# Optimization experiments

Hardware: AMD Instinct MI355X
Metric: run time of the kernel (lower is better)

## Reference

```python
import jax, jax.numpy as jnp
import numpy as np

B, L, D, H = 4, 2048, 1024, 16
DH = D // H

def setup_inputs() -> dict:
    key = jax.random.key(0)
    ks = jax.random.split(key, 9)
    s = 1.0 / np.sqrt(D)
    x = jax.random.normal(ks[0], (B, L, D), dtype=jnp.float32)
    Wq = jax.random.uniform(ks[1], (D, D), jnp.float32, -s, s)
    bq = jax.random.uniform(ks[2], (D,), jnp.float32, -s, s)
    Wk = jax.random.uniform(ks[3], (D, D), jnp.float32, -s, s)
    bk = jax.random.uniform(ks[4], (D,), jnp.float32, -s, s)
    Wv = jax.random.uniform(ks[5], (D, D), jnp.float32, -s, s)
    bv = jax.random.uniform(ks[6], (D,), jnp.float32, -s, s)
    Wo = jax.random.uniform(ks[7], (D, D), jnp.float32, -s, s)
    bo = jax.random.uniform(ks[8], (D,), jnp.float32, -s, s)
    mask = jnp.tril(jnp.ones((L, L), dtype=jnp.int32))[None, None]  # [1,1,L,L] causal
    return {"x": x, "Wq": Wq, "bq": bq, "Wk": Wk, "bk": bk, "Wv": Wv, "bv": bv,
            "Wo": Wo, "bo": bo, "mask": mask}

def reference(x, Wq, bq, Wk, bk, Wv, bv, Wo, bo, mask):
    # projections (torch Linear: x @ W.T + b; here W stored transposed already as [D,D])
    q = (x @ Wq + bq).reshape(B, L, H, DH).transpose(0, 2, 1, 3)  # [B,H,L,Dh]
    k = (x @ Wk + bk).reshape(B, L, H, DH).transpose(0, 2, 1, 3)
    v = (x @ Wv + bv).reshape(B, L, H, DH).transpose(0, 2, 1, 3)
    scores = jnp.einsum('bhqd,bhkd->bhqk', q, k) / jnp.sqrt(jnp.float32(DH))
    scores = jnp.where(mask == 0, -jnp.inf, scores)
    attn = jax.nn.softmax(scores, axis=-1)
    out = jnp.einsum('bhqk,bhkd->bhqd', attn, v)  # [B,H,L,Dh]
    out = out.transpose(0, 2, 1, 3).reshape(B, L, D)
    return out @ Wo + bo
```

## Files before the change

### kernel.cpp

```cpp
#include <hip/hip_runtime.h>
#include <hip/hip_bf16.h>


typedef __bf16 bf16;
typedef __bf16 bf16x4 __attribute__((ext_vector_type(4)));
typedef __bf16 bf16x8 __attribute__((ext_vector_type(8)));
typedef float f32x4 __attribute__((ext_vector_type(4)));

#define DEV static __device__ __forceinline__

constexpr int B = 4, L = 2048, D = 1024, H = 16, DH = 64;
constexpr int BL = B * L;
constexpr int GM = 8192, GK = 1024;
constexpr int BKg = 64;

typedef __attribute__((address_space(1))) const void* gptr1;
typedef __attribute__((address_space(3))) void* lptr3;

DEV void load_lds16(const bf16* g, bf16* l) {
  __builtin_amdgcn_global_load_lds((gptr1)g, (lptr3)l, 16, 0, 0);
}

DEV f32x4 mfma(bf16x8 a, bf16x8 b, f32x4 c) {
  return __builtin_amdgcn_mfma_f32_16x16x32_bf16(a, b, c, 0, 0, 0);
}

DEV float scrub(float v) { return (v == v) ? v : 0.f; }
DEV float max3f(float a, float b, float c) { return fmaxf(fmaxf(a, b), c); }

__global__ void sniff_k(const unsigned short* __restrict__ xr, int* flag) {
  __shared__ int cnt;
  if (threadIdx.x == 0) cnt = 0;
  __syncthreads();
  int local = 0;
  for (int i = threadIdx.x; i < 4096; i += 256) {
    const unsigned short u = xr[2 * i];
    const int e = (u >> 7) & 0xFF;
    if (e >= 0x70 && e <= 0x85) local++;
  }
  atomicAdd(&cnt, local);
  __syncthreads();
  if (threadIdx.x == 0) *flag = (cnt > 2048) ? 1 : 0;
}

__global__ __launch_bounds__(256) void cvt_x_k(const void* __restrict__ src,
                                               bf16* __restrict__ dst,
                                               const int* __restrict__ flag, int n) {
  const bool isbf = (*flag != 0);
  const int stride = gridDim.x * blockDim.x * 8;
  for (int idx = (blockIdx.x * blockDim.x + threadIdx.x) * 8; idx < n; idx += stride) {
    bf16x8 o;
    if (isbf) {
      bf16x8 v = *(const bf16x8*)((const bf16*)src + idx);
      #pragma unroll
      for (int j = 0; j < 8; ++j) o[j] = (bf16)scrub((float)v[j]);
    } else {
      const float* s = (const float*)src + idx;
      #pragma unroll
      for (int j = 0; j < 8; ++j) o[j] = (bf16)scrub(s[j]);
    }
    *(bf16x8*)&dst[idx] = o;
  }
}

__global__ __launch_bounds__(256) void wtrans_cvt4_k(const void* __restrict__ W0,
                                                     const void* __restrict__ W1,
                                                     const void* __restrict__ W2,
                                                     const void* __restrict__ W3,
                                                     bf16* __restrict__ dstBase,
                                                     const int* __restrict__ flag) {
  __shared__ bf16 t[32][33];
  const bool isbf = (*flag != 0);
  const int z = blockIdx.z;
  const void* src = (z == 0) ? W0 : (z == 1) ? W1 : (z == 2) ? W2 : W3;
  bf16* dst = dstBase + (size_t)z * D * D;
  const int bx = blockIdx.x * 32, by = blockIdx.y * 32;
  const int tx = threadIdx.x & 31, ty = threadIdx.x >> 5;
  for (int i = ty; i < 32; i += 8) {
    const size_t off = (size_t)(by + i) * D + bx + tx;
    const float v = isbf ? (float)((const bf16*)src)[off] : ((const float*)src)[off];
    t[i][tx] = (bf16)scrub(v);
  }
  __syncthreads();
  for (int i = ty; i < 32; i += 8)
    dst[(size_t)(bx + i) * D + by + tx] = t[tx][i];
}

__global__ __launch_bounds__(256) void qkv_gemm_k(const bf16* __restrict__ A,
                                                  const bf16* __restrict__ Bt,
                                                  const void* __restrict__ bq,
                                                  const void* __restrict__ bk,
                                                  const void* __restrict__ bv,
                                                  bf16* __restrict__ Q,
                                                  bf16* __restrict__ Kk,
                                                  bf16* __restrict__ VT,
                                                  const int* __restrict__ flag) {
  __shared__ __align__(16) bf16 As[128 * BKg];
  __shared__ __align__(16) bf16 Bs[128 * BKg];
  const bool isbf = (*flag != 0);
  const int wg = blockIdx.x;
  const int local = wg >> 3;
  const int mt = (wg & 7) * 8 + (local & 7);
  const int nt = local >> 3;
  const int m0 = mt * 128, n0 = nt * 128;
  const int buf = n0 >> 10, nloc = n0 & 1023;
  const void* bias = (buf == 0) ? bq : (buf == 1) ? bk : bv;
  const float scale = (buf == 0) ? 0.18033688011111f : 1.0f;

  const int tid = threadIdx.x, wave = tid >> 6, lane = tid & 63;
  const int wr = wave >> 1, wc = wave & 1;
  const int quad = lane >> 4, l16 = lane & 15;
  const int srow = lane >> 3;
  const int scol = ((lane ^ srow) & 7) * 8;
  const int l7 = l16 & 7;
  const int s0 = ((quad ^ l7) * 8);
  const int s1 = s0 ^ 32;

  f32x4 acc[4][4] = {};

  for (int k0 = 0; k0 < GK; k0 += BKg) {
    for (int c = wave; c < 16; c += 4) {
      load_lds16(A  + (size_t)(m0 + c * 8 + srow) * GK + k0 + scol, &As[c * 512]);
      load_lds16(Bt + (size_t)(n0 + c * 8 + srow) * GK + k0 + scol, &Bs[c * 512]);
    }
    __syncthreads();
    #pragma unroll
    for (int kk = 0; kk < BKg; kk += 32) {
      const int sk = kk ? s1 : s0;
      bf16x8 af[4], bfr[4];
      #pragma unroll
      for (int i = 0; i < 4; ++i)
        af[i] = *(const bf16x8*)&As[(wr * 64 + i * 16 + l16) * BKg + sk];
      #pragma unroll
      for (int i = 0; i < 4; ++i)
        bfr[i] = *(const bf16x8*)&Bs[(wc * 64 + i * 16 + l16) * BKg + sk];
      #pragma unroll
      for (int mi = 0; mi < 4; ++mi)
        #pragma unroll
        for (int ni = 0; ni < 4; ++ni)
          acc[mi][ni] = mfma(af[mi], bfr[ni], acc[mi][ni]);
    }
    __syncthreads();
  }

  if (buf < 2) {
    bf16* Cb = (buf == 0) ? Q : Kk;
    #pragma unroll
    for (int ni = 0; ni < 4; ++ni) {
      const int col = nloc + wc * 64 + ni * 16 + l16;
      const float bv2 = isbf ? (float)((const bf16*)bias)[col] : ((const float*)bias)[col];
      #pragma unroll
      for (int mi = 0; mi < 4; ++mi)
        #pragma unroll
        for (int r = 0; r < 4; ++r) {
          const int row = m0 + wr * 64 + mi * 16 + quad * 4 + r;
          Cb[(size_t)row * D + col] = (bf16)((acc[mi][ni][r] + bv2) * scale);
        }
    }
  } else {
    #pragma unroll
    for (int ni = 0; ni < 4; ++ni) {
      const int col = nloc + wc * 64 + ni * 16 + l16;
      const int h = col >> 6, d = col & 63;
      const float bv2 = isbf ? (float)((const bf16*)bias)[col] : ((const float*)bias)[col];
      #pragma unroll
      for (int mi = 0; mi < 4; ++mi) {
        const int row = m0 + wr * 64 + mi * 16 + quad * 4;
        const int bb = row >> 11, l = row & 2047;
        const int pos = (l & ~31) + 4 * ((l >> 4) & 1) + 8 * ((l >> 2) & 3);
        bf16x4 pk;
        #pragma unroll
        for (int r = 0; r < 4; ++r) pk[r] = (bf16)(acc[mi][ni][r] + bv2);
        *(bf16x4*)&VT[((size_t)(bb * 16 + h) * 64 + d) * L + pos] = pk;
      }
    }
  }
}

__global__ __launch_bounds__(256) void gemm_bt_k(const bf16* __restrict__ A,
                                                 const bf16* __restrict__ Bt,
                                                 const void* __restrict__ bias,
                                                 void* __restrict__ C,
                                                 const int* __restrict__ flag) {
  __shared__ __align__(16) bf16 As[128 * BKg];
  __shared__ __align__(16) bf16 Bs[128 * BKg];
  const bool isbf = (*flag != 0);
  const int wg = blockIdx.x;
  const int local = wg >> 3;
  const int mt = (wg & 7) * 8 + (local & 7);
  const int nt = local >> 3;
  const int m0 = mt * 128, n0 = nt * 128;
  const int tid = threadIdx.x, wave = tid >> 6, lane = tid & 63;
  const int wr = wave >> 1, wc = wave & 1;
  const int quad = lane >> 4, l16 = lane & 15;
  const int srow = lane >> 3;
  const int scol = ((lane ^ srow) & 7) * 8;
  const int l7 = l16 & 7;
  const int s0 = ((quad ^ l7) * 8);
  const int s1 = s0 ^ 32;

  f32x4 acc[4][4] = {};

  for (int k0 = 0; k0 < GK; k0 += BKg) {
    for (int c = wave; c < 16; c += 4) {
      load_lds16(A  + (size_t)(m0 + c * 8 + srow) * GK + k0 + scol, &As[c * 512]);
      load_lds16(Bt + (size_t)(n0 + c * 8 + srow) * GK + k0 + scol, &Bs[c * 512]);
    }
    __syncthreads();
    #pragma unroll
    for (int kk = 0; kk < BKg; kk += 32) {
      const int sk = kk ? s1 : s0;
      bf16x8 af[4], bfr[4];
      #pragma unroll
      for (int i = 0; i < 4; ++i)
        af[i] = *(const bf16x8*)&As[(wr * 64 + i * 16 + l16) * BKg + sk];
      #pragma unroll
      for (int i = 0; i < 4; ++i)
        bfr[i] = *(const bf16x8*)&Bs[(wc * 64 + i * 16 + l16) * BKg + sk];
      #pragma unroll
      for (int mi = 0; mi < 4; ++mi)
        #pragma unroll
        for (int ni = 0; ni < 4; ++ni)
          acc[mi][ni] = mfma(af[mi], bfr[ni], acc[mi][ni]);
    }
    __syncthreads();
  }

  bf16* Cb = (bf16*)C;
  float* Cf = (float*)C;
  #pragma unroll
  for (int ni = 0; ni < 4; ++ni) {
    const int col = n0 + wc * 64 + ni * 16 + l16;
    const float bv = isbf ? (float)((const bf16*)bias)[col] : ((const float*)bias)[col];
    #pragma unroll
    for (int mi = 0; mi < 4; ++mi)
      #pragma unroll
      for (int r = 0; r < 4; ++r) {
        const int row = m0 + wr * 64 + mi * 16 + quad * 4 + r;
        const float v = acc[mi][ni][r] + bv;
        if (isbf) Cb[(size_t)row * D + col] = (bf16)v;
        else      Cf[(size_t)row * D + col] = v;
      }
  }
}

__global__ __launch_bounds__(256) void attn_k(bf16* QO,
                                              const bf16* __restrict__ K,
                                              const bf16* __restrict__ VT) {
  __shared__ __align__(16) bf16 Ks[2][64 * 64];
  __shared__ __align__(16) bf16 Vt[2][64 * 64];

  const int bx = blockIdx.x;
  const int qt = (L / 64 - 1) - (bx >> 6);
  const int bh = bx & 63;
  const int b = bh >> 4, h = bh & 15;
  const int tid = threadIdx.x, wave = tid >> 6, lane = tid & 63;
  const int quad = lane >> 4, l16 = lane & 15;
  const int srow = lane >> 3;
  const int scol = ((lane ^ srow) & 7) * 8;
  const int l7 = l16 & 7;
  const int s0 = ((quad ^ l7) * 8);
  const int s1 = s0 ^ 32;

  bf16* Qb = QO + (size_t)b * L * D + h * DH;
  const bf16* Kb = K + (size_t)b * L * D + h * DH;
  const bf16* VTg = VT + (size_t)bh * DH * L;

  const int qrow = qt * 64 + wave * 16 + l16;
  const bf16x8 qf0 = *(const bf16x8*)(Qb + (size_t)qrow * D + quad * 8);
  const bf16x8 qf1 = *(const bf16x8*)(Qb + (size_t)qrow * D + 32 + quad * 8);

  bf16x8 ones;
  #pragma unroll
  for (int j = 0; j < 8; ++j) ones[j] = (bf16)1.0f;

  float m_run = -INFINITY;
  f32x4 o_acc[4] = {};
  f32x4 o_sum = {};

  const int nkt = qt + 1;

  const bf16* kg0 = Kb + (size_t)(wave * 8 + srow) * D + scol;
  const bf16* kg1 = kg0 + (size_t)32 * D;
  const bf16* vg0 = VTg + (size_t)(wave * 8 + srow) * L + scol;
  const bf16* vg1 = vg0 + (size_t)32 * L;
  const int kl0 = wave * 512, kl1 = kl0 + 2048;

  load_lds16(kg0, &Ks[0][kl0]);
  load_lds16(kg1, &Ks[0][kl1]);
  load_lds16(vg0, &Vt[0][kl0]);
  load_lds16(vg1, &Vt[0][kl1]);
  kg0 += (size_t)64 * D; kg1 += (size_t)64 * D; vg0 += 64; vg1 += 64;
  __syncthreads();

  int cur = 0;
  for (int kt = 0; kt < nkt; ++kt) {
    if (kt + 1 < nkt) {
      bf16* Kn = &Ks[cur ^ 1][0];
      bf16* Vn = &Vt[cur ^ 1][0];
      load_lds16(kg0, &Kn[kl0]);
      load_lds16(kg1, &Kn[kl1]);
      load_lds16(vg0, &Vn[kl0]);
      load_lds16(vg1, &Vn[kl1]);
      kg0 += (size_t)64 * D; kg1 += (size_t)64 * D; vg0 += 64; vg1 += 64;
    }

    const bf16* Kc = &Ks[cur][0];
    const bf16* Vc = &Vt[cur][0];

    f32x4 s[4];
    #pragma unroll
    for (int sub = 0; sub < 4; ++sub) {
      bf16x8 k0 = *(const bf16x8*)&Kc[(sub * 16 + l16) * 64 + s0];
      bf16x8 k1 = *(const bf16x8*)&Kc[(sub * 16 + l16) * 64 + s1];
      f32x4 a = {};
      a = mfma(k0, qf0, a);
      a = mfma(k1, qf1, a);
      s[sub] = a;
    }

    if (kt == qt) {
      const int qloc = wave * 16 + l16;
      #pragma unroll
      for (int sub = 0; sub < 4; ++sub)
        #pragma unroll
        for (int r = 0; r < 4; ++r)
          if (sub * 16 + quad * 4 + r > qloc) s[sub][r] = -1e30f;
    }

    const float t0 = max3f(s[0][0], s[0][1], s[0][2]);
    const float t1 = max3f(s[0][3], s[1][0], s[1][1]);
    const float t2 = max3f(s[1][2], s[1][3], s[2][0]);
    const float t3 = max3f(s[2][1], s[2][2], s[2][3]);
    const float t4 = max3f(s[3][0], s[3][1], s[3][2]);
    float mx = fmaxf(max3f(t0, t1, t2), max3f(t3, t4, s[3][3]));
    mx = fmaxf(mx, __shfl_xor(mx, 16, 64));
    mx = fmaxf(mx, __shfl_xor(mx, 32, 64));

    if (!__all(mx <= m_run + 8.f)) {
      const float mn = fmaxf(m_run, mx);
      const float alpha = __builtin_amdgcn_exp2f(m_run - mn);
      m_run = mn;
      #pragma unroll
      for (int r = 0; r < 4; ++r) {
        const float ar = __shfl(alpha, quad * 4 + r, 64);
        o_sum[r] *= ar;
        #pragma unroll
        for (int db = 0; db < 4; ++db) o_acc[db][r] *= ar;
      }
    }

    bf16x8 fr0, fr1;
    #pragma unroll
    for (int r = 0; r < 4; ++r) {
      fr0[r]     = (bf16)__builtin_amdgcn_exp2f(s[0][r] - m_run);
      fr0[4 + r] = (bf16)__builtin_amdgcn_exp2f(s[1][r] - m_run);
      fr1[r]     = (bf16)__builtin_amdgcn_exp2f(s[2][r] - m_run);
      fr1[4 + r] = (bf16)__builtin_amdgcn_exp2f(s[3][r] - m_run);
    }

    o_sum = mfma(fr0, ones, o_sum);
    o_sum = mfma(fr1, ones, o_sum);
    #pragma unroll
    for (int db = 0; db < 4; ++db) {
      bf16x8 v0 = *(const bf16x8*)&Vc[(db * 16 + l16) * 64 + s0];
      bf16x8 v1 = *(const bf16x8*)&Vc[(db * 16 + l16) * 64 + s1];
      o_acc[db] = mfma(fr0, v0, o_acc[db]);
      o_acc[db] = mfma(fr1, v1, o_acc[db]);
    }

    __syncthreads();
    cur ^= 1;
  }

  #pragma unroll
  for (int r = 0; r < 4; ++r) {
    const float inv = 1.f / o_sum[r];
    const int row = qt * 64 + wave * 16 + quad * 4 + r;
    #pragma unroll
    for (int db = 0; db < 4; ++db)
      Qb[(size_t)row * D + db * 16 + l16] = (bf16)(o_acc[db][r] * inv);
  }
}

extern "C" void kernel_launch(void* const* d_in, const int* in_sizes, int n_in,
                              void* d_out, int out_size, void* d_ws, size_t ws_size,
                              hipStream_t stream) {
  const void* x  = d_in[0];
  const void* Wq = d_in[1];
  const void* bq = d_in[2];
  const void* Wk = d_in[3];
  const void* bk = d_in[4];
  const void* Wv = d_in[5];
  const void* bv = d_in[6];
  const void* Wo = d_in[7];
  const void* bo = d_in[8];

  int* flag = (int*)d_ws;
  char* p = (char*)d_ws + 4096;
  bf16* xc  = (bf16*)p;                 p += (size_t)BL * D * 2;
  bf16* WqT = (bf16*)p;                 p += (size_t)D * D * 2;
  bf16* WkT = (bf16*)p;                 p += (size_t)D * D * 2;
  bf16* WvT = (bf16*)p;                 p += (size_t)D * D * 2;
  bf16* WoT = (bf16*)p;                 p += (size_t)D * D * 2;
  bf16* Qb  = (bf16*)p;                 p += (size_t)BL * D * 2;
  bf16* Kb  = (bf16*)p;                 p += (size_t)BL * D * 2;
  bf16* VTb = (bf16*)p;

  sniff_k<<<1, 256, 0, stream>>>((const unsigned short*)x, flag);

  cvt_x_k<<<1024, 256, 0, stream>>>(x, xc, flag, BL * D);
  wtrans_cvt4_k<<<dim3(32, 32, 4), 256, 0, stream>>>(Wq, Wk, Wv, Wo, WqT, flag);

  qkv_gemm_k<<<dim3(1536), 256, 0, stream>>>(
      xc, WqT, bq, bk, bv, Qb, Kb, VTb, flag);

  attn_k<<<dim3((L / 64) * B * H), 256, 0, stream>>>(Qb, Kb, VTb);

  gemm_bt_k<<<dim3(512), 256, 0, stream>>>(Qb, WoT, bo, d_out, flag);
}
```

Baseline: 267.6 us.

## Merge prep kernels, use plain 2D GEMM grids, raise MFMA priority in attention

Fuses the x conversion and the weight transpose-convert into one launch by adding a fifth z-slice of blocks that converts x, which saves one kernel launch. Replaces the swizzled 1D tile mapping in both GEMMs with a plain 2D grid (x over M tiles, y over N tiles). This drops the grouped ordering that helped L2 reuse. Also wraps the attention MFMA sections in s_setprio to favour matrix-issue waves.

```diff
diff --git a/kernel.cpp b/kernel.cpp
--- a/kernel.cpp
+++ b/kernel.cpp
@@ -43,47 +43,47 @@
   if (threadIdx.x == 0) *flag = (cnt > 2048) ? 1 : 0;
 }
 
-__global__ __launch_bounds__(256) void cvt_x_k(const void* __restrict__ src,
-                                               bf16* __restrict__ dst,
-                                               const int* __restrict__ flag, int n) {
-  const bool isbf = (*flag != 0);
-  const int stride = gridDim.x * blockDim.x * 8;
-  for (int idx = (blockIdx.x * blockDim.x + threadIdx.x) * 8; idx < n; idx += stride) {
-    bf16x8 o;
-    if (isbf) {
-      bf16x8 v = *(const bf16x8*)((const bf16*)src + idx);
-      #pragma unroll
-      for (int j = 0; j < 8; ++j) o[j] = (bf16)scrub((float)v[j]);
-    } else {
-      const float* s = (const float*)src + idx;
-      #pragma unroll
-      for (int j = 0; j < 8; ++j) o[j] = (bf16)scrub(s[j]);
-    }
-    *(bf16x8*)&dst[idx] = o;
-  }
-}
-
-__global__ __launch_bounds__(256) void wtrans_cvt4_k(const void* __restrict__ W0,
-                                                     const void* __restrict__ W1,
-                                                     const void* __restrict__ W2,
-                                                     const void* __restrict__ W3,
-                                                     bf16* __restrict__ dstBase,
-                                                     const int* __restrict__ flag) {
+__global__ __launch_bounds__(256) void prep_k(const void* __restrict__ W0,
+                                              const void* __restrict__ W1,
+                                              const void* __restrict__ W2,
+                                              const void* __restrict__ W3,
+                                              bf16* __restrict__ dstBase,
+                                              const void* __restrict__ x,
+                                              bf16* __restrict__ xc,
+                                              const int* __restrict__ flag, int n) {
   __shared__ bf16 t[32][33];
   const bool isbf = (*flag != 0);
   const int z = blockIdx.z;
-  const void* src = (z == 0) ? W0 : (z == 1) ? W1 : (z == 2) ? W2 : W3;
-  bf16* dst = dstBase + (size_t)z * D * D;
-  const int bx = blockIdx.x * 32, by = blockIdx.y * 32;
-  const int tx = threadIdx.x & 31, ty = threadIdx.x >> 5;
-  for (int i = ty; i < 32; i += 8) {
-    const size_t off = (size_t)(by + i) * D + bx + tx;
-    const float v = isbf ? (float)((const bf16*)src)[off] : ((const float*)src)[off];
-    t[i][tx] = (bf16)scrub(v);
-  }
-  __syncthreads();
-  for (int i = ty; i < 32; i += 8)
-    dst[(size_t)(bx + i) * D + by + tx] = t[tx][i];
+  if (z < 4) {
+    const void* src = (z == 0) ? W0 : (z == 1) ? W1 : (z == 2) ? W2 : W3;
+    bf16* dst = dstBase + (size_t)z * D * D;
+    const int bx = blockIdx.x * 32, by = blockIdx.y * 32;
+    const int tx = threadIdx.x & 31, ty = threadIdx.x >> 5;
+    for (int i = ty; i < 32; i += 8) {
+      const size_t off = (size_t)(by + i) * D + bx + tx;
+      const float v = isbf ? (float)((const bf16*)src)[off] : ((const float*)src)[off];
+      t[i][tx] = (bf16)scrub(v);
+    }
+    __syncthreads();
+    for (int i = ty; i < 32; i += 8)
+      dst[(size_t)(bx + i) * D + by + tx] = t[tx][i];
+  } else {
+    const int bid = blockIdx.y * 32 + blockIdx.x;
+    const int stride = 1024 * 256 * 8;
+    for (int idx = (bid * 256 + (int)threadIdx.x) * 8; idx < n; idx += stride) {
+      bf16x8 o;
+      if (isbf) {
+        bf16x8 v = *(const bf16x8*)((const bf16*)x + idx);
+        #pragma unroll
+        for (int j = 0; j < 8; ++j) o[j] = (bf16)scrub((float)v[j]);
+      } else {
+        const float* s = (const float*)x + idx;
+        #pragma unroll
+        for (int j = 0; j < 8; ++j) o[j] = (bf16)scrub(s[j]);
+      }
+      *(bf16x8*)&xc[idx] = o;
+    }
+  }
 }
 
 __global__ __launch_bounds__(256) void qkv_gemm_k(const bf16* __restrict__ A,
@@ -98,11 +98,7 @@
   __shared__ __align__(16) bf16 As[128 * BKg];
   __shared__ __align__(16) bf16 Bs[128 * BKg];
   const bool isbf = (*flag != 0);
-  const int wg = blockIdx.x;
-  const int local = wg >> 3;
-  const int mt = (wg & 7) * 8 + (local & 7);
-  const int nt = local >> 3;
-  const int m0 = mt * 128, n0 = nt * 128;
+  const int m0 = blockIdx.x * 128, n0 = blockIdx.y * 128;
   const int buf = n0 >> 10, nloc = n0 & 1023;
   const void* bias = (buf == 0) ? bq : (buf == 1) ? bk : bv;
   const float scale = (buf == 0) ? 0.18033688011111f : 1.0f;
@@ -185,11 +181,7 @@
   __shared__ __align__(16) bf16 As[128 * BKg];
   __shared__ __align__(16) bf16 Bs[128 * BKg];
   const bool isbf = (*flag != 0);
-  const int wg = blockIdx.x;
-  const int local = wg >> 3;
-  const int mt = (wg & 7) * 8 + (local & 7);
-  const int nt = local >> 3;
-  const int m0 = mt * 128, n0 = nt * 128;
+  const int m0 = blockIdx.x * 128, n0 = blockIdx.y * 128;
   const int tid = threadIdx.x, wave = tid >> 6, lane = tid & 63;
   const int wr = wave >> 1, wc = wave & 1;
   const int quad = lane >> 4, l16 = lane & 15;
@@ -309,6 +301,7 @@
     const bf16* Vc = &Vt[cur][0];
 
     f32x4 s[4];
+    __builtin_amdgcn_s_setprio(1);
     #pragma unroll
     for (int sub = 0; sub < 4; ++sub) {
       bf16x8 k0 = *(const bf16x8*)&Kc[(sub * 16 + l16) * 64 + s0];
@@ -318,6 +311,7 @@
       a = mfma(k1, qf1, a);
       s[sub] = a;
     }
+    __builtin_amdgcn_s_setprio(0);
 
     if (kt == qt) {
       const int qloc = wave * 16 + l16;
@@ -359,6 +353,7 @@
       fr1[4 + r] = (bf16)__builtin_amdgcn_exp2f(s[3][r] - m_run);
     }
 
+    __builtin_amdgcn_s_setprio(1);
     o_sum = mfma(fr0, ones, o_sum);
     o_sum = mfma(fr1, ones, o_sum);
     #pragma unroll
@@ -368,6 +363,7 @@
       o_acc[db] = mfma(fr0, v0, o_acc[db]);
       o_acc[db] = mfma(fr1, v1, o_acc[db]);
     }
+    __builtin_amdgcn_s_setprio(0);
 
     __syncthreads();
     cur ^= 1;
@@ -409,13 +405,12 @@
 
   sniff_k<<<1, 256, 0, stream>>>((const unsigned short*)x, flag);
 
-  cvt_x_k<<<1024, 256, 0, stream>>>(x, xc, flag, BL * D);
-  wtrans_cvt4_k<<<dim3(32, 32, 4), 256, 0, stream>>>(Wq, Wk, Wv, Wo, WqT, flag);
-
-  qkv_gemm_k<<<dim3(1536), 256, 0, stream>>>(
+  prep_k<<<dim3(32, 32, 5), 256, 0, stream>>>(Wq, Wk, Wv, Wo, WqT, x, xc, flag, BL * D);
+
+  qkv_gemm_k<<<dim3(GM / 128, 3072 / 128), 256, 0, stream>>>(
       xc, WqT, bq, bk, bv, Qb, Kb, VTb, flag);
 
   attn_k<<<dim3((L / 64) * B * H), 256, 0, stream>>>(Qb, Kb, VTb);
 
-  gemm_bt_k<<<dim3(512), 256, 0, stream>>>(Qb, WoT, bo, d_out, flag);
-}
+  gemm_bt_k<<<dim3(GM / 128, D / 128), 256, 0, stream>>>(Qb, WoT, bo, d_out, flag);
+}
```

New measurement: 267.2 us. No clear change (-0.2%).
